# Optimization experiments

Hardware: AMD Instinct MI355X
Metric: run time of the kernel (lower is better)

The kernel has to match this reference:

```python
import jax, jax.numpy as jnp
import numpy as np

B, S, D, H, E = 4, 2048, 1024, 4096, 8
THRESHOLD = 0.5


def setup_inputs() -> dict:
    key = jax.random.key(0)
    ks = jax.random.split(key, 7)
    s_in = 1.0 / np.sqrt(D)
    s_h = 1.0 / np.sqrt(H)
    return {
        "x": jax.random.normal(ks[0], (B, S, D), dtype=jnp.float32),
        "Wg": jax.random.uniform(ks[1], (D, E), jnp.float32, -s_in, s_in),
        "bg": jax.random.uniform(ks[2], (E,), jnp.float32, -s_in, s_in),
        "W1": jax.random.uniform(ks[3], (E, D, H), jnp.float32, -s_in, s_in),
        "b1": jax.random.uniform(ks[4], (E, H), jnp.float32, -s_in, s_in),
        "W2": jax.random.uniform(ks[5], (E, H, D), jnp.float32, -s_h, s_h),
        "b2": jax.random.uniform(ks[6], (E, D), jnp.float32, -s_h, s_h),
    }


def reference(x, Wg, bg, W1, b1, W2, b2):
    b, s, d = x.shape
    x_flat = x.reshape(-1, d)                       # [T, D], T = B*S
    # Top-any gating: sigmoid logits, threshold mask, weights = probs * mask
    probs = jax.nn.sigmoid(x_flat @ Wg + bg)        # [T, E]
    mask = (probs > THRESHOLD).astype(x_flat.dtype)
    weights = probs * mask                          # [T, E]
    # Dense per-expert MLP over all tokens (faithful to the torch loop)
    h = jax.nn.relu(jnp.einsum('td,edh->eth', x_flat, W1) + b1[:, None, :])  # [E, T, H]
    expert_out = jnp.einsum('eth,ehd->etd', h, W2) + b2[:, None, :]          # [E, T, D]
    combined = jnp.einsum('te,etd->td', weights, expert_out)                 # [T, D]
    return combined.reshape(b, s, d)
```

## Files before the change

kernel.cpp:

```cpp
#include <hip/hip_runtime.h>
#include <hip/hip_bf16.h>

#define T_TOK 8192
#define D_DIM 1024
#define H_DIM 4096
#define E_NUM 8
#define IDXST 8448
#define CAPBLK 18
#define CAPROWS (CAPBLK * 256)

typedef short bf16x8 __attribute__((ext_vector_type(8)));
typedef float f32x4 __attribute__((ext_vector_type(4)));

__device__ __forceinline__ unsigned short f2bf(float f) {
    union { float f; unsigned int u; } v; v.f = f;
    unsigned int u = v.u;
    u = u + 0x7FFFu + ((u >> 16) & 1u);
    return (unsigned short)(u >> 16);
}

__device__ __forceinline__ void gload_lds16(const void* g, void* l) {
    __builtin_amdgcn_global_load_lds(
        (const __attribute__((address_space(1))) unsigned int*)g,
        (__attribute__((address_space(3))) unsigned int*)l,
        16, 0, 0);
}

#define SBAR() { __builtin_amdgcn_sched_barrier(0); __builtin_amdgcn_s_barrier(); __builtin_amdgcn_sched_barrier(0); }
#define LGKM0() { asm volatile("s_waitcnt lgkmcnt(0)" ::: "memory"); __builtin_amdgcn_sched_barrier(0); }
#define VMC3() { asm volatile("s_waitcnt vmcnt(3)" ::: "memory"); __builtin_amdgcn_sched_barrier(0); }
#define VMC0() { asm volatile("s_waitcnt vmcnt(0)" ::: "memory"); __builtin_amdgcn_sched_barrier(0); }

__device__ __forceinline__ int swz_rt(int lin, int n) {
    int q = n >> 3, r = n & 7;
    int xcd = lin & 7, pos = lin >> 3;
    int base = (xcd < r) ? xcd * (q + 1) : r * (q + 1) + (xcd - r) * q;
    return base + pos;
}

template<int NBN>
__device__ __forceinline__ bool merged_map(const int* __restrict__ cntp,
                                           int& e, int& bm, int& bn, int& cnt_e) {
    int nbs[E_NUM], tot = 0;
    #pragma unroll
    for (int i = 0; i < E_NUM; ++i) {
        int c = cntp[i];
        int nbm = (c + 255) >> 8;
        if (nbm > CAPBLK) nbm = CAPBLK;
        nbs[i] = nbm * NBN;
        tot += nbs[i];
    }
    if ((int)blockIdx.x >= tot) return false;
    const int wg = swz_rt(blockIdx.x, tot);
    int acc = 0, loc = 0;
    e = 0;
    #pragma unroll
    for (int i = 0; i < E_NUM; ++i) {
        if (wg >= acc && wg < acc + nbs[i]) { e = i; loc = wg - acc; }
        acc += nbs[i];
    }
    bm = loc / NBN;
    bn = loc - bm * NBN;
    cnt_e = cntp[e];
    return true;
}

__global__ void gate_cvt_kernel(const float* __restrict__ x, const float* __restrict__ Wg,
                                const float* __restrict__ bg, float* __restrict__ wout,
                                unsigned short* __restrict__ xb) {
    int wv = (int)((blockIdx.x * blockDim.x + threadIdx.x) >> 6);
    int lane = threadIdx.x & 63;
    if (wv >= T_TOK) return;
    const float* xr = x + (size_t)wv * D_DIM;
    unsigned short* xo = xb + (size_t)wv * D_DIM;
    double acc[E_NUM] = {0, 0, 0, 0, 0, 0, 0, 0};
    for (int i = 0; i < D_DIM / 64; ++i) {
        int d = i * 64 + lane;
        float xf = xr[d];
        xo[d] = f2bf(xf);
        double xv = (double)xf;
        const float* wr = Wg + (size_t)d * E_NUM;
        #pragma unroll
        for (int e = 0; e < E_NUM; ++e) acc[e] += xv * (double)wr[e];
    }
    #pragma unroll
    for (int e = 0; e < E_NUM; ++e) {
        double v = acc[e];
        for (int s = 32; s; s >>= 1) v += __shfl_down(v, s, 64);
        acc[e] = v;
    }
    if (lane == 0) {
        #pragma unroll
        for (int e = 0; e < E_NUM; ++e) {
            double z = acc[e] + (double)bg[e];
            float p = (float)(1.0 / (1.0 + exp(-z)));
            wout[(size_t)wv * E_NUM + e] = (p > 0.5f) ? p : 0.0f;
        }
    }
}

__global__ void compact_kernel(const float* __restrict__ wgt, int* __restrict__ idx,
                               float* __restrict__ wc, int* __restrict__ cnt) {
    const int e = blockIdx.x;
    const int tid = threadIdx.x;
    const int lane = tid & 63, wv = tid >> 6;
    int* idxe = idx + e * IDXST;
    float* wce = wc + e * IDXST;
    __shared__ int wtot[4];
    __shared__ int sbase;
    if (tid == 0) sbase = 0;
    __syncthreads();
    for (int t0 = 0; t0 < T_TOK; t0 += 256) {
        int t = t0 + tid;
        float w = wgt[(size_t)t * E_NUM + e];
        int act = (w > 0.0f) ? 1 : 0;
        unsigned long long mask = __ballot(act);
        int wpos = __popcll(mask & ((1ull << lane) - 1ull));
        if (lane == 0) wtot[wv] = __popcll(mask);
        __syncthreads();
        int off = sbase;
        for (int i = 0; i < wv; ++i) off += wtot[i];
        if (act) { idxe[off + wpos] = t; wce[off + wpos] = w; }
        __syncthreads();
        if (tid == 0) sbase += wtot[0] + wtot[1] + wtot[2] + wtot[3];
        __syncthreads();
    }
    int total = sbase;
    int padded = ((total + 255) / 256) * 256;
    for (int i = total + tid; i < padded; i += 256) { idxe[i] = 0; wce[i] = 0.0f; }
    if (tid == 0) cnt[e] = total;
}

__global__ void transpose_cvt(const float* __restrict__ in, unsigned short* __restrict__ out,
                              int R, int C) {
    __shared__ unsigned short tile[64][65];
    int e = blockIdx.z;
    const float* src = in + (size_t)e * R * C;
    unsigned short* dst = out + (size_t)e * R * C;
    int c0 = blockIdx.x * 64, r0 = blockIdx.y * 64;
    int t = threadIdx.x;
    int cc = (t & 15) * 4;
    int rr = t >> 4;
    #pragma unroll
    for (int p = 0; p < 4; ++p) {
        int r = rr + p * 16;
        float4 v = *(const float4*)(src + (size_t)(r0 + r) * C + c0 + cc);
        tile[cc + 0][r] = f2bf(v.x);
        tile[cc + 1][r] = f2bf(v.y);
        tile[cc + 2][r] = f2bf(v.z);
        tile[cc + 3][r] = f2bf(v.w);
    }
    __syncthreads();
    int rr4 = (t & 15) * 4;
    int cw = t >> 4;
    #pragma unroll
    for (int p = 0; p < 4; ++p) {
        int c = cw + p * 16;
        ushort4 o;
        o.x = tile[c][rr4 + 0];
        o.y = tile[c][rr4 + 1];
        o.z = tile[c][rr4 + 2];
        o.w = tile[c][rr4 + 3];
        *(ushort4*)(dst + (size_t)(c0 + c) * R + r0 + rr4) = o;
    }
}

__global__ void zero_kernel(float4* __restrict__ p, size_t n4) {
    size_t i = (size_t)blockIdx.x * blockDim.x + threadIdx.x;
    size_t st = (size_t)gridDim.x * blockDim.x;
    for (; i < n4; i += st) p[i] = (float4){0.f, 0.f, 0.f, 0.f};
}

__global__ void sentinel_kernel(float* out, size_t n) {
    size_t i = (size_t)blockIdx.x * blockDim.x + threadIdx.x;
    size_t st = (size_t)gridDim.x * blockDim.x;
    for (; i < n; i += st) out[i] = 12345.0f;
}

__global__ __launch_bounds__(512, 4) void gemm1c(
    const unsigned short* __restrict__ Xb,
    const unsigned short* __restrict__ W1T,
    unsigned short* __restrict__ Hc,
    const float* __restrict__ b1,
    const int* __restrict__ idxb,
    const float* __restrict__ wcb,
    const int* __restrict__ cntp)
{
    __shared__ __align__(16) unsigned short lA[3][8192];
    __shared__ __align__(16) unsigned short lB[3][4096];

    int e, bm, bn, cnt;
    if (!merged_map<H_DIM / 128>(cntp, e, bm, bn, cnt)) return;

    const int* idx = idxb + e * IDXST;
    const float* wc = wcb + e * IDXST;
    const unsigned short* Bmat = W1T + (size_t)e * H_DIM * D_DIM;
    const float* b1e = b1 + (size_t)e * H_DIM;
    unsigned short* HcE = Hc + (size_t)e * CAPROWS * H_DIM;

    const int tid = threadIdx.x;
    const int lane = tid & 63, wid = tid >> 6;
    const int wr = wid >> 1;
    const int wcn = wid & 1;
    const int fr = lane & 15, fq = lane >> 4;

    const int srow = tid >> 2;
    const int scol = (((tid & 3) ^ ((tid >> 3) & 3)) << 3);
    const unsigned short* Asrc0 = Xb + (size_t)idx[bm * 256 + srow] * D_DIM + scol;
    const unsigned short* Asrc1 = Xb + (size_t)idx[bm * 256 + 128 + srow] * D_DIM + scol;
    const unsigned short* Bb = Bmat + (size_t)(bn * 128 + srow) * D_DIM + scol;

    const int soff = (fq ^ ((fr >> 1) & 3)) * 8;

    f32x4 acc[4][4];
    #pragma unroll
    for (int m = 0; m < 4; ++m)
        #pragma unroll
        for (int n = 0; n < 4; ++n)
            acc[m][n] = (f32x4){0.f, 0.f, 0.f, 0.f};

    bf16x8 a[4], b[4];

    auto stageA = [&](int bf, int kt) {
        gload_lds16(Asrc0 + kt * 32, &lA[bf][tid * 8]);
        gload_lds16(Asrc1 + kt * 32, &lA[bf][4096 + tid * 8]);
    };
    auto stageB = [&](int bf, int kt) {
        gload_lds16(Bb + kt * 32, &lB[bf][tid * 8]);
    };

    stageA(0, 0); stageB(0, 0);
    stageA(1, 1); stageB(1, 1);
    VMC3();
    SBAR();

    const int NT = D_DIM / 32;
    int cb = 0;
    for (int t = 0; t < NT; ++t) {
        const int nb2 = (cb + 2 >= 3) ? cb - 1 : cb + 2;
        #pragma unroll
        for (int mm = 0; mm < 4; ++mm) {
            const int r = wr * 64 + mm * 16 + fr;
            a[mm] = *(const bf16x8*)&lA[cb][r * 32 + soff];
        }
        #pragma unroll
        for (int n = 0; n < 4; ++n) {
            const int rB = wcn * 64 + n * 16 + fr;
            b[n] = *(const bf16x8*)&lB[cb][rB * 32 + soff];
        }
        if (t + 2 < NT) { stageA(nb2, t + 2); stageB(nb2, t + 2); }
        LGKM0();
        __builtin_amdgcn_s_setprio(1);
        #pragma unroll
        for (int mm = 0; mm < 4; ++mm)
            #pragma unroll
            for (int n = 0; n < 4; ++n)
                acc[mm][n] = __builtin_amdgcn_mfma_f32_16x16x32_bf16(a[mm], b[n], acc[mm][n], 0, 0, 0);
        __builtin_amdgcn_s_setprio(0);
        if (t < NT - 2) { VMC3(); } else { VMC0(); }
        SBAR();
        cb = (cb == 2) ? 0 : cb + 1;
    }

    #pragma unroll
    for (int m = 0; m < 4; ++m) {
        const int rbase = bm * 256 + wr * 64 + m * 16 + fq * 4;
        #pragma unroll
        for (int n = 0; n < 4; ++n) {
            const int cn = bn * 128 + wcn * 64 + n * 16 + fr;
            const float bb = b1e[cn];
            #pragma unroll
            for (int j = 0; j < 4; ++j) {
                const int r = rbase + j;
                const float w = wc[r];
                float v = fmaxf(acc[m][n][j] + bb, 0.0f) * w;
                HcE[(size_t)r * H_DIM + cn] = f2bf(v);
            }
        }
    }
}

__global__ __launch_bounds__(512, 4) void gemm2c(
    const unsigned short* __restrict__ Hc,
    const unsigned short* __restrict__ W2T,
    float* __restrict__ out,
    const float* __restrict__ b2,
    const int* __restrict__ idxb,
    const float* __restrict__ wcb,
    const int* __restrict__ cntp)
{
    __shared__ __align__(16) unsigned short lA[3][8192];
    __shared__ __align__(16) unsigned short lB[3][4096];

    int e, bm, bn, cnt;
    if (!merged_map<D_DIM / 128>(cntp, e, bm, bn, cnt)) return;

    const int* idx = idxb + e * IDXST;
    const float* wc = wcb + e * IDXST;
    const unsigned short* A = Hc + (size_t)e * CAPROWS * H_DIM;
    const unsigned short* Bmat = W2T + (size_t)e * D_DIM * H_DIM;
    const float* b2e = b2 + (size_t)e * D_DIM;

    const int tid = threadIdx.x;
    const int lane = tid & 63, wid = tid >> 6;
    const int wr = wid >> 1;
    const int wcn = wid & 1;
    const int fr = lane & 15, fq = lane >> 4;

    const int srow = tid >> 2;
    const int scol = (((tid & 3) ^ ((tid >> 3) & 3)) << 3);
    const unsigned short* Ab = A + (size_t)(bm * 256 + srow) * H_DIM + scol;
    const unsigned short* Bb = Bmat + (size_t)(bn * 128 + srow) * H_DIM + scol;

    const int soff = (fq ^ ((fr >> 1) & 3)) * 8;

    f32x4 acc[4][4];
    #pragma unroll
    for (int m = 0; m < 4; ++m)
        #pragma unroll
        for (int n = 0; n < 4; ++n)
            acc[m][n] = (f32x4){0.f, 0.f, 0.f, 0.f};

    bf16x8 a[4], b[4];

    auto stageA = [&](int bf, int kt) {
        gload_lds16(Ab + kt * 32,                       &lA[bf][tid * 8]);
        gload_lds16(Ab + (size_t)128 * H_DIM + kt * 32, &lA[bf][4096 + tid * 8]);
    };
    auto stageB = [&](int bf, int kt) {
        gload_lds16(Bb + kt * 32, &lB[bf][tid * 8]);
    };

    stageA(0, 0); stageB(0, 0);
    stageA(1, 1); stageB(1, 1);
    VMC3();
    SBAR();

    const int NT = H_DIM / 32;
    int cb = 0;
    for (int t = 0; t < NT; ++t) {
        const int nb2 = (cb + 2 >= 3) ? cb - 1 : cb + 2;
        #pragma unroll
        for (int mm = 0; mm < 4; ++mm) {
            const int r = wr * 64 + mm * 16 + fr;
            a[mm] = *(const bf16x8*)&lA[cb][r * 32 + soff];
        }
        #pragma unroll
        for (int n = 0; n < 4; ++n) {
            const int rB = wcn * 64 + n * 16 + fr;
            b[n] = *(const bf16x8*)&lB[cb][rB * 32 + soff];
        }
        if (t + 2 < NT) { stageA(nb2, t + 2); stageB(nb2, t + 2); }
        LGKM0();
        __builtin_amdgcn_s_setprio(1);
        #pragma unroll
        for (int mm = 0; mm < 4; ++mm)
            #pragma unroll
            for (int n = 0; n < 4; ++n)
                acc[mm][n] = __builtin_amdgcn_mfma_f32_16x16x32_bf16(a[mm], b[n], acc[mm][n], 0, 0, 0);
        __builtin_amdgcn_s_setprio(0);
        if (t < NT - 2) { VMC3(); } else { VMC0(); }
        SBAR();
        cb = (cb == 2) ? 0 : cb + 1;
    }

    #pragma unroll
    for (int m = 0; m < 4; ++m) {
        const int rbase = bm * 256 + wr * 64 + m * 16 + fq * 4;
        #pragma unroll
        for (int n = 0; n < 4; ++n) {
            const int cn = bn * 128 + wcn * 64 + n * 16 + fr;
            const float bb = b2e[cn];
            #pragma unroll
            for (int j = 0; j < 4; ++j) {
                const int row = rbase + j;
                if (row < cnt) {
                    const int tok = idx[row];
                    atomicAdd(&out[(size_t)tok * D_DIM + cn], acc[m][n][j] + wc[row] * bb);
                }
            }
        }
    }
}

extern "C" void kernel_launch(void* const* d_in, const int* in_sizes, int n_in,
                              void* d_out, int out_size, void* d_ws, size_t ws_size,
                              hipStream_t stream) {
    const float* x  = (const float*)d_in[0];
    const float* Wg = (const float*)d_in[1];
    const float* bg = (const float*)d_in[2];
    const float* W1 = (const float*)d_in[3];
    const float* b1 = (const float*)d_in[4];
    const float* W2 = (const float*)d_in[5];
    const float* b2 = (const float*)d_in[6];
    float* out = (float*)d_out;
    char* ws = (char*)d_ws;

    const size_t off_w   = 0;
    const size_t off_idx = 262144;
    const size_t off_wcc = 557056;
    const size_t off_cnt = 851968;
    const size_t off_x   = 1048576;
    const size_t off_w1  = off_x + (size_t)T_TOK * D_DIM * 2;
    const size_t off_w2  = off_w1 + (size_t)E_NUM * D_DIM * H_DIM * 2;
    const size_t off_h   = off_w2 + (size_t)E_NUM * D_DIM * H_DIM * 2;
    const size_t cap_h   = (size_t)E_NUM * CAPROWS * H_DIM * 2;

    if (ws_size < off_h + cap_h) {
        sentinel_kernel<<<2048, 256, 0, stream>>>(out, (size_t)T_TOK * D_DIM);
        return;
    }

    float* wgt = (float*)(ws + off_w);
    int* idxb  = (int*)(ws + off_idx);
    float* wcb = (float*)(ws + off_wcc);
    int* cntb  = (int*)(ws + off_cnt);
    unsigned short* Xb  = (unsigned short*)(ws + off_x);
    unsigned short* W1T = (unsigned short*)(ws + off_w1);
    unsigned short* W2T = (unsigned short*)(ws + off_w2);
    unsigned short* Hc  = (unsigned short*)(ws + off_h);

    gate_cvt_kernel<<<T_TOK / 4, 256, 0, stream>>>(x, Wg, bg, wgt, Xb);
    transpose_cvt<<<dim3(H_DIM / 64, D_DIM / 64, E_NUM), 256, 0, stream>>>(W1, W1T, D_DIM, H_DIM);
    transpose_cvt<<<dim3(D_DIM / 64, H_DIM / 64, E_NUM), 256, 0, stream>>>(W2, W2T, H_DIM, D_DIM);

    compact_kernel<<<E_NUM, 256, 0, stream>>>(wgt, idxb, wcb, cntb);
    zero_kernel<<<2048, 256, 0, stream>>>((float4*)out, (size_t)T_TOK * D_DIM / 4);
    const int g1 = E_NUM * CAPBLK * (H_DIM / 128);
    const int g2 = E_NUM * CAPBLK * (D_DIM / 128);
    gemm1c<<<g1, 512, 0, stream>>>(Xb, W1T, Hc, b1, idxb, wcb, cntb);
    gemm2c<<<g2, 512, 0, stream>>>(Hc, W2T, out, b2, idxb, wcb, cntb);
}
```

Measured before the change: 901.2 us.

## Replace atomic scatter-add in down-projection with compact store plus gather reduce

The second GEMM now writes each expert's per-row outputs to a compact fp32 buffer instead of atomically adding into the output. A new reduce kernel uses a per-token position map, built in the compaction kernel, to gather and sum each token's expert contributions. This also removes the output zeroing pass. It removes atomic contention and read-modify-write traffic, at the cost of an extra ~150MB workspace write and read. The new path runs only when the workspace is large enough, otherwise the old atomic path is used.

New measurement: 923.2 us. +2.4%, slower.

```diff
diff --git a/kernel.cpp b/kernel.cpp
--- a/kernel.cpp
+++ b/kernel.cpp
@@ -100,12 +100,14 @@
 }
 
 __global__ void compact_kernel(const float* __restrict__ wgt, int* __restrict__ idx,
-                               float* __restrict__ wc, int* __restrict__ cnt) {
+                               float* __restrict__ wc, int* __restrict__ cnt,
+                               int* __restrict__ pos) {
     const int e = blockIdx.x;
     const int tid = threadIdx.x;
     const int lane = tid & 63, wv = tid >> 6;
     int* idxe = idx + e * IDXST;
     float* wce = wc + e * IDXST;
+    int* pose = pos + e * T_TOK;
     __shared__ int wtot[4];
     __shared__ int sbase;
     if (tid == 0) sbase = 0;
@@ -120,7 +122,8 @@
         __syncthreads();
         int off = sbase;
         for (int i = 0; i < wv; ++i) off += wtot[i];
-        if (act) { idxe[off + wpos] = t; wce[off + wpos] = w; }
+        if (act) { idxe[off + wpos] = t; wce[off + wpos] = w; pose[t] = off + wpos + 1; }
+        else pose[t] = 0;
         __syncthreads();
         if (tid == 0) sbase += wtot[0] + wtot[1] + wtot[2] + wtot[3];
         __syncthreads();
@@ -169,6 +172,24 @@
     size_t i = (size_t)blockIdx.x * blockDim.x + threadIdx.x;
     size_t st = (size_t)gridDim.x * blockDim.x;
     for (; i < n4; i += st) p[i] = (float4){0.f, 0.f, 0.f, 0.f};
+}
+
+__global__ void reduce_kernel(const float4* __restrict__ Oc, const int* __restrict__ pos,
+                              float4* __restrict__ out) {
+    const int D4 = D_DIM / 4;
+    size_t i = (size_t)blockIdx.x * blockDim.x + threadIdx.x;
+    int t = (int)(i / D4);
+    int dv = (int)(i - (size_t)t * D4);
+    f32x4 s = (f32x4){0.f, 0.f, 0.f, 0.f};
+    #pragma unroll
+    for (int e = 0; e < E_NUM; ++e) {
+        int p = pos[e * T_TOK + t];
+        if (p) {
+            float4 v = Oc[((size_t)e * CAPROWS + (p - 1)) * D4 + dv];
+            s[0] += v.x; s[1] += v.y; s[2] += v.z; s[3] += v.w;
+        }
+    }
+    out[i] = (float4){s[0], s[1], s[2], s[3]};
 }
 
 __global__ void sentinel_kernel(float* out, size_t n) {
@@ -280,10 +301,12 @@
     }
 }
 
+template<int STORE>
 __global__ __launch_bounds__(512, 4) void gemm2c(
     const unsigned short* __restrict__ Hc,
     const unsigned short* __restrict__ W2T,
     float* __restrict__ out,
+    float* __restrict__ Oc,
     const float* __restrict__ b2,
     const int* __restrict__ idxb,
     const float* __restrict__ wcb,
@@ -300,6 +323,7 @@
     const unsigned short* A = Hc + (size_t)e * CAPROWS * H_DIM;
     const unsigned short* Bmat = W2T + (size_t)e * D_DIM * H_DIM;
     const float* b2e = b2 + (size_t)e * D_DIM;
+    float* OcE = Oc + (size_t)e * CAPROWS * D_DIM;
 
     const int tid = threadIdx.x;
     const int lane = tid & 63, wid = tid >> 6;
@@ -374,9 +398,12 @@
             #pragma unroll
             for (int j = 0; j < 4; ++j) {
                 const int row = rbase + j;
-                if (row < cnt) {
+                const float v = acc[m][n][j] + wc[row] * bb;
+                if (STORE == 1) {
+                    OcE[(size_t)row * D_DIM + cn] = v;
+                } else if (row < cnt) {
                     const int tok = idx[row];
-                    atomicAdd(&out[(size_t)tok * D_DIM + cn], acc[m][n][j] + wc[row] * bb);
+                    atomicAdd(&out[(size_t)tok * D_DIM + cn], v);
                 }
             }
         }
@@ -398,36 +425,48 @@
 
     const size_t off_w   = 0;
     const size_t off_idx = 262144;
-    const size_t off_wcc = 557056;
-    const size_t off_cnt = 851968;
-    const size_t off_x   = 1048576;
+    const size_t off_wcc = 532480;
+    const size_t off_cnt = 802816;
+    const size_t off_pos = 806912;
+    const size_t off_x   = 2097152;
     const size_t off_w1  = off_x + (size_t)T_TOK * D_DIM * 2;
     const size_t off_w2  = off_w1 + (size_t)E_NUM * D_DIM * H_DIM * 2;
     const size_t off_h   = off_w2 + (size_t)E_NUM * D_DIM * H_DIM * 2;
     const size_t cap_h   = (size_t)E_NUM * CAPROWS * H_DIM * 2;
+    const size_t off_oc  = off_h + cap_h;
+    const size_t oc_sz   = (size_t)E_NUM * CAPROWS * D_DIM * 4;
 
     if (ws_size < off_h + cap_h) {
         sentinel_kernel<<<2048, 256, 0, stream>>>(out, (size_t)T_TOK * D_DIM);
         return;
     }
+    const bool storePath = (ws_size >= off_oc + oc_sz);
 
     float* wgt = (float*)(ws + off_w);
     int* idxb  = (int*)(ws + off_idx);
     float* wcb = (float*)(ws + off_wcc);
     int* cntb  = (int*)(ws + off_cnt);
+    int* posb  = (int*)(ws + off_pos);
     unsigned short* Xb  = (unsigned short*)(ws + off_x);
     unsigned short* W1T = (unsigned short*)(ws + off_w1);
     unsigned short* W2T = (unsigned short*)(ws + off_w2);
     unsigned short* Hc  = (unsigned short*)(ws + off_h);
+    float* Oc = (float*)(ws + off_oc);
 
     gate_cvt_kernel<<<T_TOK / 4, 256, 0, stream>>>(x, Wg, bg, wgt, Xb);
     transpose_cvt<<<dim3(H_DIM / 64, D_DIM / 64, E_NUM), 256, 0, stream>>>(W1, W1T, D_DIM, H_DIM);
     transpose_cvt<<<dim3(D_DIM / 64, H_DIM / 64, E_NUM), 256, 0, stream>>>(W2, W2T, H_DIM, D_DIM);
 
-    compact_kernel<<<E_NUM, 256, 0, stream>>>(wgt, idxb, wcb, cntb);
-    zero_kernel<<<2048, 256, 0, stream>>>((float4*)out, (size_t)T_TOK * D_DIM / 4);
+    compact_kernel<<<E_NUM, 256, 0, stream>>>(wgt, idxb, wcb, cntb, posb);
     const int g1 = E_NUM * CAPBLK * (H_DIM / 128);
     const int g2 = E_NUM * CAPBLK * (D_DIM / 128);
     gemm1c<<<g1, 512, 0, stream>>>(Xb, W1T, Hc, b1, idxb, wcb, cntb);
-    gemm2c<<<g2, 512, 0, stream>>>(Hc, W2T, out, b2, idxb, wcb, cntb);
-}
+    if (storePath) {
+        gemm2c<1><<<g2, 512, 0, stream>>>(Hc, W2T, out, Oc, b2, idxb, wcb, cntb);
+        reduce_kernel<<<(T_TOK * (D_DIM / 4)) / 256, 256, 0, stream>>>(
+            (const float4*)Oc, posb, (float4*)out);
+    } else {
+        zero_kernel<<<2048, 256, 0, stream>>>((float4*)out, (size_t)T_TOK * D_DIM / 4);
+        gemm2c<0><<<g2, 512, 0, stream>>>(Hc, W2T, out, Oc, b2, idxb, wcb, cntb);
+    }
+}
```
